# Kernel optimization log

Measured on AMD Instinct MI355X. Metric: run time of the kernel, lower is better.

## Reference

```python
import jax, jax.numpy as jnp
import numpy as np

B, N, E = 2, 50000, 800000
INP, KEY, VAL = 128, 64, 128
LN_EPS = 1e-5


def setup_inputs() -> dict:
    key = jax.random.key(0)
    ks = jax.random.split(key, 12)
    s_in = 1.0 / np.sqrt(INP).astype(np.float32)
    s_val = 1.0 / np.sqrt(VAL).astype(np.float32)
    return {
        "x": jax.random.normal(ks[0], (B, N, INP), jnp.float32),
        "conn_vals": jax.random.uniform(ks[1], (E,), jnp.float32),
        "k_w": jax.random.normal(ks[2], (INP, KEY), jnp.float32) * s_in,
        "k_b": jax.random.normal(ks[3], (KEY,), jnp.float32) * 0.01,
        "v_w": jax.random.normal(ks[4], (INP, VAL), jnp.float32) * s_in,
        "v_b": jax.random.normal(ks[5], (VAL,), jnp.float32) * 0.01,
        "out_w": jax.random.normal(ks[6], (VAL, VAL), jnp.float32) * s_val,
        "out_b": jax.random.normal(ks[7], (VAL,), jnp.float32) * 0.01,
        "ln_g": jnp.ones((VAL,), jnp.float32),
        "ln_b": jnp.zeros((VAL,), jnp.float32),
        "rows": jax.random.randint(ks[8], (E,), 0, N),
        "cols": jax.random.randint(ks[9], (E,), 0, N),
    }


def reference(x, conn_vals, k_w, k_b, v_w, v_b, out_w, out_b, ln_g, ln_b, rows, cols):
    # x: [B, N, INP]; edge list (rows -> receivers, cols -> senders)
    keys = x @ k_w + k_b                      # [B, N, KEY]
    values = x @ v_w + v_b                    # [B, N, VAL]

    # weights[i, j, b] = conn[i, j] * sum_k keys[b, j, k]
    ksum = keys.sum(axis=-1)                  # [B, N]
    score = conn_vals[:, None] * ksum[:, cols].T   # [E, B]

    # sparse softmax over dim=1 (senders j), per receiver row i and batch b,
    # restricted to specified (edge) entries only
    m = jax.ops.segment_max(score, rows, num_segments=N)     # [N, B]
    m = jnp.where(jnp.isfinite(m), m, 0.0)                   # empty rows
    ex = jnp.exp(score - m[rows])                            # [E, B]
    denom = jax.ops.segment_sum(ex, rows, num_segments=N)    # [N, B]
    w = ex / jnp.where(denom == 0.0, 1.0, denom)[rows]       # [E, B]

    # output[i, b, :] = sum_j w[i, j, b] * values[b, j, :]
    vals_g = jnp.swapaxes(values[:, cols], 0, 1)             # [E, B, VAL]
    msgs = w[:, :, None] * vals_g                            # [E, B, VAL]
    agg = jax.ops.segment_sum(msgs, rows, num_segments=N)    # [N, B, VAL]

    h = jnp.transpose(agg, (1, 0, 2)) @ out_w + out_b        # [B, N, VAL]
    h = jax.nn.silu(h)

    mu = h.mean(axis=-1, keepdims=True)
    var = ((h - mu) ** 2).mean(axis=-1, keepdims=True)
    out = (h - mu) / jnp.sqrt(var + LN_EPS) * ln_g + ln_b
    return out
```

## Files before the change

### kernel.cpp

```cpp
#include <hip/hip_runtime.h>
#include <hip/hip_bf16.h>

#define NB    2
#define NNODE 50000
#define NEDGE 800000
#define INPD  128
#define KEYD  64
#define VALD  128
#define MTOT  (NB * NNODE)
#define VBLK  3125
#define EPT   16
#define SBLK  ((NEDGE + 256 * EPT - 1) / (256 * EPT))
#define ECAP  80

typedef __attribute__((ext_vector_type(8))) short bf16x8;
typedef __attribute__((ext_vector_type(4))) float f32x4;

__device__ __forceinline__ unsigned short f2bf(float f) {
    unsigned u = __float_as_uint(f);
    u += 0x7FFFu + ((u >> 16) & 1u);
    return (unsigned short)(u >> 16);
}

__global__ void prep_kernel(const float* __restrict__ kw, const float* __restrict__ kb,
                            const float* __restrict__ vw, const float* __restrict__ ow,
                            float* __restrict__ kwsum,
                            unsigned short* __restrict__ vwT, unsigned short* __restrict__ owT,
                            int* __restrict__ cursor) {
    int bid = blockIdx.x, tid = threadIdx.x;
    if (bid < 64) {
        int idx = bid * 256 + tid;
        int n = idx >> 7, k = idx & 127;
        vwT[idx] = f2bf(vw[k * VALD + n]);
    } else if (bid < 128) {
        int idx = (bid - 64) * 256 + tid;
        int n = idx >> 7, k = idx & 127;
        owT[idx] = f2bf(ow[k * VALD + n]);
    } else if (bid == 128) {
        if (tid < INPD) {
            float s = 0.f;
            for (int j = 0; j < KEYD; ++j) s += kw[tid * KEYD + j];
            kwsum[tid] = s;
        }
        if (tid == 0) {
            float s = 0.f;
            for (int j = 0; j < KEYD; ++j) s += kb[j];
            kwsum[INPD] = s;
        }
    } else {
        int idx = (bid - 129) * 256 + tid;
        if (idx < NNODE) cursor[idx] = idx * ECAP;
    }
}

__global__ __launch_bounds__(256, 8)
void values_build_kernel(const float* __restrict__ x, const float* __restrict__ vb,
                         const float* __restrict__ kwsum,
                         const unsigned short* __restrict__ vwT,
                         const int* __restrict__ rows_e, const int* __restrict__ cols_e,
                         const float* __restrict__ conn,
                         uint2* __restrict__ values_pk, float* __restrict__ ksum,
                         int* __restrict__ cursor, uint2* __restrict__ edge_s) {
    __shared__ unsigned short xs[32 * 136];
    __shared__ unsigned short pk[16 * 264];
    int tid = threadIdx.x;
    if (blockIdx.x < SBLK) {
        int base = blockIdx.x * 256 + tid;
#pragma unroll
        for (int k = 0; k < EPT; ++k) {
            int e = base + k * (SBLK * 256);
            if (e < NEDGE) {
                int r = rows_e[e];
                int o = atomicAdd(&cursor[r], 1);
                if (o < r * ECAP + ECAP) {
                    unsigned long long pkd =
                        (unsigned long long)(unsigned)cols_e[e]
                        | ((unsigned long long)__float_as_uint(conn[e]) << 32);
                    __builtin_nontemporal_store(
                        pkd, (unsigned long long*)&edge_s[o]);
                }
            }
        }
        return;
    }
    int node0 = (blockIdx.x - SBLK) * 16;

    {
        int row = tid >> 4;
        int cseg = tid & 15;
        const float4* p0 = (const float4*)(x + (size_t)(node0 + row) * INPD) + cseg * 2;
        const float4* p1 = (const float4*)(x + (size_t)(NNODE + node0 + row) * INPD) + cseg * 2;
        float4 u0 = p0[0], u1 = p0[1];
        float4 w0 = p1[0], w1 = p1[1];
        const float4* kwp = (const float4*)kwsum + cseg * 2;
        float4 ka = kwp[0], kc = kwp[1];
        float kp0 = u0.x * ka.x + u0.y * ka.y + u0.z * ka.z + u0.w * ka.w
                  + u1.x * kc.x + u1.y * kc.y + u1.z * kc.z + u1.w * kc.w;
        float kp1 = w0.x * ka.x + w0.y * ka.y + w0.z * ka.z + w0.w * ka.w
                  + w1.x * kc.x + w1.y * kc.y + w1.z * kc.z + w1.w * kc.w;
#pragma unroll
        for (int o = 1; o < 16; o <<= 1) {
            kp0 += __shfl_xor(kp0, o);
            kp1 += __shfl_xor(kp1, o);
        }
        if (cseg == 0) {
            float kb = kwsum[INPD];
            ksum[node0 + row] = kp0 + kb;
            ksum[NNODE + node0 + row] = kp1 + kb;
        }
        union { unsigned short h[8]; uint4 q; } a, b;
        a.h[0] = f2bf(u0.x); a.h[1] = f2bf(u0.y); a.h[2] = f2bf(u0.z); a.h[3] = f2bf(u0.w);
        a.h[4] = f2bf(u1.x); a.h[5] = f2bf(u1.y); a.h[6] = f2bf(u1.z); a.h[7] = f2bf(u1.w);
        b.h[0] = f2bf(w0.x); b.h[1] = f2bf(w0.y); b.h[2] = f2bf(w0.z); b.h[3] = f2bf(w0.w);
        b.h[4] = f2bf(w1.x); b.h[5] = f2bf(w1.y); b.h[6] = f2bf(w1.z); b.h[7] = f2bf(w1.w);
        *(uint4*)(xs + row * 136 + cseg * 8) = a.q;
        *(uint4*)(xs + (16 + row) * 136 + cseg * 8) = b.q;
    }
    __syncthreads();

    int wave = tid >> 6, lane = tid & 63;
    int m = lane & 15, quad = lane >> 4;
    int n0 = wave * 32;
    f32x4 acc00 = {0.f, 0.f, 0.f, 0.f};
    f32x4 acc01 = {0.f, 0.f, 0.f, 0.f};
    f32x4 acc10 = {0.f, 0.f, 0.f, 0.f};
    f32x4 acc11 = {0.f, 0.f, 0.f, 0.f};
    const unsigned short* r0 = xs + m * 136;
    const unsigned short* r1 = xs + (16 + m) * 136;
    const unsigned short* bw0 = vwT + (size_t)(n0 + m) * INPD;
    const unsigned short* bw1 = vwT + (size_t)(n0 + 16 + m) * INPD;
#pragma unroll
    for (int kk = 0; kk < 4; ++kk) {
        int k0 = kk * 32 + quad * 8;
        bf16x8 A0 = *(const bf16x8*)(r0 + k0);
        bf16x8 A1 = *(const bf16x8*)(r1 + k0);
        bf16x8 B0 = *(const bf16x8*)(bw0 + k0);
        bf16x8 B1 = *(const bf16x8*)(bw1 + k0);
        acc00 = __builtin_amdgcn_mfma_f32_16x16x32_bf16(A0, B0, acc00, 0, 0, 0);
        acc01 = __builtin_amdgcn_mfma_f32_16x16x32_bf16(A0, B1, acc01, 0, 0, 0);
        acc10 = __builtin_amdgcn_mfma_f32_16x16x32_bf16(A1, B0, acc10, 0, 0, 0);
        acc11 = __builtin_amdgcn_mfma_f32_16x16x32_bf16(A1, B1, acc11, 0, 0, 0);
    }
    int c0 = n0 + m, c1 = n0 + 16 + m;
    float vb0 = vb[c0], vb1 = vb[c1];
    int p0 = (c0 >> 1) * 4 + (c0 & 1);
    int p1 = (c1 >> 1) * 4 + (c1 & 1);
#pragma unroll
    for (int r = 0; r < 4; ++r) {
        int nl = quad * 4 + r;
        pk[nl * 264 + p0]     = f2bf(acc00[r] + vb0);
        pk[nl * 264 + p0 + 2] = f2bf(acc10[r] + vb0);
        pk[nl * 264 + p1]     = f2bf(acc01[r] + vb1);
        pk[nl * 264 + p1 + 2] = f2bf(acc11[r] + vb1);
    }
    __syncthreads();
    {
        int node = tid >> 4, chunk = tid & 15;
        uint4 q0 = *(const uint4*)(pk + node * 264 + chunk * 8);
        uint4 q1 = *(const uint4*)(pk + node * 264 + (chunk + 16) * 8);
        uint4* dst = (uint4*)((char*)values_pk + (size_t)node0 * 512) + node * 32;
        dst[chunk] = q0;
        dst[chunk + 16] = q1;
    }
}

__global__ __launch_bounds__(256)
void aggregate_kernel(const int* __restrict__ cursor,
                      const uint2* __restrict__ edge_s,
                      const float* __restrict__ ksum,
                      const uint2* __restrict__ values_pk,
                      unsigned short* __restrict__ agg_bf) {
    int wave = threadIdx.x >> 6, lane = threadIdx.x & 63;
    int wid = blockIdx.x * 4 + wave;
    for (int rr = 0; rr < 2; ++rr) {
        int i = wid * 2 + rr;
        if (i >= NNODE) break;
        int start = i * ECAP;
        int len = min(cursor[i] - start, ECAP);
        float acc00 = 0.f, acc01 = 0.f, acc10 = 0.f, acc11 = 0.f;
        if (len > 0) {
            if (len <= 64) {
                float ex0 = 0.f, ex1 = 0.f; int colv = 0;
                if (lane < len) {
                    uint2 e = edge_s[start + lane];
                    colv = (int)e.x;
                    float cv = __uint_as_float(e.y);
                    ex0 = __expf(cv * ksum[colv]);
                    ex1 = __expf(cv * ksum[NNODE + colv]);
                }
                float s0 = ex0, s1 = ex1;
#pragma unroll
                for (int o = 1; o < 64; o <<= 1) { s0 += __shfl_xor(s0, o); s1 += __shfl_xor(s1, o); }
                float inv0 = 1.0f / s0, inv1 = 1.0f / s1;
                int p = 0;
                for (; p + 3 < len; p += 4) {
                    int c0 = __shfl(colv, p),     c1 = __shfl(colv, p + 1);
                    int c2 = __shfl(colv, p + 2), c3 = __shfl(colv, p + 3);
                    float wa0 = __shfl(ex0, p) * inv0,     wb0 = __shfl(ex1, p) * inv1;
                    float wa1 = __shfl(ex0, p + 1) * inv0, wb1 = __shfl(ex1, p + 1) * inv1;
                    float wa2 = __shfl(ex0, p + 2) * inv0, wb2 = __shfl(ex1, p + 2) * inv1;
                    float wa3 = __shfl(ex0, p + 3) * inv0, wb3 = __shfl(ex1, p + 3) * inv1;
                    uint2 v0 = values_pk[(size_t)c0 * 64 + lane];
                    uint2 v1 = values_pk[(size_t)c1 * 64 + lane];
                    uint2 v2 = values_pk[(size_t)c2 * 64 + lane];
                    uint2 v3 = values_pk[(size_t)c3 * 64 + lane];
                    acc00 += wa0 * __uint_as_float(v0.x << 16) + wa1 * __uint_as_float(v1.x << 16)
                           + wa2 * __uint_as_float(v2.x << 16) + wa3 * __uint_as_float(v3.x << 16);
                    acc01 += wa0 * __uint_as_float(v0.x & 0xFFFF0000u) + wa1 * __uint_as_float(v1.x & 0xFFFF0000u)
                           + wa2 * __uint_as_float(v2.x & 0xFFFF0000u) + wa3 * __uint_as_float(v3.x & 0xFFFF0000u);
                    acc10 += wb0 * __uint_as_float(v0.y << 16) + wb1 * __uint_as_float(v1.y << 16)
                           + wb2 * __uint_as_float(v2.y << 16) + wb3 * __uint_as_float(v3.y << 16);
                    acc11 += wb0 * __uint_as_float(v0.y & 0xFFFF0000u) + wb1 * __uint_as_float(v1.y & 0xFFFF0000u)
                           + wb2 * __uint_as_float(v2.y & 0xFFFF0000u) + wb3 * __uint_as_float(v3.y & 0xFFFF0000u);
                }
                for (; p < len; ++p) {
                    int c = __shfl(colv, p);
                    float w0 = __shfl(ex0, p) * inv0;
                    float w1 = __shfl(ex1, p) * inv1;
                    uint2 v = values_pk[(size_t)c * 64 + lane];
                    acc00 += w0 * __uint_as_float(v.x << 16);
                    acc01 += w0 * __uint_as_float(v.x & 0xFFFF0000u);
                    acc10 += w1 * __uint_as_float(v.y << 16);
                    acc11 += w1 * __uint_as_float(v.y & 0xFFFF0000u);
                }
            } else {
                float s0 = 0.f, s1 = 0.f;
                for (int basep = 0; basep < len; basep += 64) {
                    int q = basep + lane;
                    if (q < len) {
                        uint2 e = edge_s[start + q];
                        int c = (int)e.x;
                        float cv = __uint_as_float(e.y);
                        s0 += __expf(cv * ksum[c]);
                        s1 += __expf(cv * ksum[NNODE + c]);
                    }
                }
#pragma unroll
                for (int o = 1; o < 64; o <<= 1) { s0 += __shfl_xor(s0, o); s1 += __shfl_xor(s1, o); }
                float inv0 = 1.0f / s0, inv1 = 1.0f / s1;
                for (int p = 0; p < len; ++p) {
                    uint2 e = edge_s[start + p];
                    int c = (int)e.x;
                    float cv = __uint_as_float(e.y);
                    float w0 = __expf(cv * ksum[c]) * inv0;
                    float w1 = __expf(cv * ksum[NNODE + c]) * inv1;
                    uint2 v = values_pk[(size_t)c * 64 + lane];
                    acc00 += w0 * __uint_as_float(v.x << 16);
                    acc01 += w0 * __uint_as_float(v.x & 0xFFFF0000u);
                    acc10 += w1 * __uint_as_float(v.y << 16);
                    acc11 += w1 * __uint_as_float(v.y & 0xFFFF0000u);
                }
            }
        }
        unsigned o0 = ((unsigned)f2bf(acc01) << 16) | (unsigned)f2bf(acc00);
        unsigned o1 = ((unsigned)f2bf(acc11) << 16) | (unsigned)f2bf(acc10);
        ((unsigned*)(agg_bf + (size_t)i * VALD))[lane] = o0;
        ((unsigned*)(agg_bf + (size_t)(NNODE + i) * VALD))[lane] = o1;
    }
}

__global__ __launch_bounds__(256)
void out_kernel(const unsigned short* __restrict__ agg_bf,
                const unsigned short* __restrict__ owT,
                const float* __restrict__ ob,
                const float* __restrict__ lng, const float* __restrict__ lnb,
                float* __restrict__ out) {
    __shared__ float hs[16][VALD + 2];
    __shared__ float ps[16][16];
    __shared__ float psq[16][16];
    __shared__ float mu_s[16], rs_s[16];
    int m0 = blockIdx.x * 16;
    int tid = threadIdx.x;
    int wave = tid >> 6, lane = tid & 63;
    int m = lane & 15, quad = lane >> 4;
    int n0 = wave * 32;
    f32x4 a0 = {0.f, 0.f, 0.f, 0.f}, a1 = {0.f, 0.f, 0.f, 0.f};
    const unsigned short* arow = agg_bf + (size_t)(m0 + m) * VALD;
#pragma unroll
    for (int kk = 0; kk < 4; ++kk) {
        int k0 = kk * 32 + quad * 8;
        bf16x8 af = *(const bf16x8*)(arow + k0);
        bf16x8 b0 = *(const bf16x8*)(owT + (size_t)(n0 + m) * VALD + k0);
        bf16x8 b1 = *(const bf16x8*)(owT + (size_t)(n0 + 16 + m) * VALD + k0);
        a0 = __builtin_amdgcn_mfma_f32_16x16x32_bf16(af, b0, a0, 0, 0, 0);
        a1 = __builtin_amdgcn_mfma_f32_16x16x32_bf16(af, b1, a1, 0, 0, 0);
    }
#pragma unroll
    for (int r = 0; r < 4; ++r) {
        int row = quad * 4 + r;
        {
            int col = n0 + m;
            float h = a0[r] + ob[col];
            hs[row][col] = h / (1.f + __expf(-h));
        }
        {
            int col = n0 + 16 + m;
            float h = a1[r] + ob[col];
            hs[row][col] = h / (1.f + __expf(-h));
        }
    }
    __syncthreads();
    {
        int row = tid >> 4, seg = tid & 15;
        float s = 0.f, q = 0.f;
#pragma unroll
        for (int j = 0; j < 8; ++j) {
            float v = hs[row][seg * 8 + j];
            s += v; q += v * v;
        }
        ps[row][seg] = s; psq[row][seg] = q;
    }
    __syncthreads();
    if (tid < 16) {
        float s = 0.f, q = 0.f;
#pragma unroll
        for (int j = 0; j < 16; ++j) { s += ps[tid][j]; q += psq[tid][j]; }
        float mu = s * (1.f / 128.f);
        float var = q * (1.f / 128.f) - mu * mu;
        mu_s[tid] = mu;
        rs_s[tid] = rsqrtf(var + 1e-5f);
    }
    __syncthreads();
#pragma unroll
    for (int j = 0; j < 8; ++j) {
        int e = tid + 256 * j;
        int row = e >> 7, col = e & 127;
        out[(size_t)(m0 + row) * VALD + col] =
            (hs[row][col] - mu_s[row]) * rs_s[row] * lng[col] + lnb[col];
    }
}

extern "C" void kernel_launch(void* const* d_in, const int* in_sizes, int n_in,
                              void* d_out, int out_size, void* d_ws, size_t ws_size,
                              hipStream_t stream) {
    (void)in_sizes; (void)n_in; (void)out_size; (void)ws_size;
    const float* x    = (const float*)d_in[0];
    const float* conn = (const float*)d_in[1];
    const float* kw   = (const float*)d_in[2];
    const float* kb   = (const float*)d_in[3];
    const float* vw   = (const float*)d_in[4];
    const float* vb   = (const float*)d_in[5];
    const float* ow   = (const float*)d_in[6];
    const float* ob   = (const float*)d_in[7];
    const float* lng  = (const float*)d_in[8];
    const float* lnb  = (const float*)d_in[9];
    const int* rows   = (const int*)d_in[10];
    const int* cols   = (const int*)d_in[11];
    float* out        = (float*)d_out;

    char* w = (char*)d_ws;
    auto alloc = [&](size_t bytes) {
        char* p = w;
        w += (bytes + 255) & ~(size_t)255;
        return p;
    };
    uint2* values_pk       = (uint2*)alloc((size_t)NNODE * 512);
    unsigned short* agg_bf = (unsigned short*)alloc((size_t)MTOT * VALD * 2);
    float* ksum   = (float*)alloc((size_t)MTOT * 4);
    float* kwsum  = (float*)alloc(256 * 4);
    int*   cursor = (int*)alloc((size_t)NNODE * 4);
    uint2* edge_s = (uint2*)alloc((size_t)NNODE * ECAP * 8);
    unsigned short* vwT = (unsigned short*)alloc((size_t)INPD * VALD * 2);
    unsigned short* owT = (unsigned short*)alloc((size_t)VALD * VALD * 2);

    prep_kernel<<<129 + 196, 256, 0, stream>>>(kw, kb, vw, ow, kwsum, vwT, owT, cursor);
    values_build_kernel<<<SBLK + VBLK, 256, 0, stream>>>(
        x, vb, kwsum, vwT, rows, cols, conn, values_pk, ksum, cursor, edge_s);
    aggregate_kernel<<<(NNODE + 7) / 8, 256, 0, stream>>>(
        cursor, edge_s, ksum, values_pk, agg_bf);
    out_kernel<<<MTOT / 16, 256, 0, stream>>>(agg_bf, owT, ob, lng, lnb, out);
}
```

Before: 264.2 us.

## Fuse aggregation with output projection, SiLU and LayerNorm via shared memory

Merges the aggregate and out kernels so each block aggregates 8 nodes for both batches, stages the bf16 results in LDS as a 16-row tile, then runs the MFMA projection, SiLU and LayerNorm directly. This removes the global round-trip of the aggregated tensor (write then read of roughly 51 MB in bf16) and one kernel launch. In exchange, each block now holds extra LDS and a block-wide barrier after the irregular gather phase, which may reduce occupancy and let slow waves stall the whole block.

Result: faster. 246.1 us, median of 2 (-6.9%).

```diff
diff --git a/kernel.cpp b/kernel.cpp
--- a/kernel.cpp
+++ b/kernel.cpp
@@ -165,16 +165,26 @@
 }
 
 __global__ __launch_bounds__(256)
-void aggregate_kernel(const int* __restrict__ cursor,
-                      const uint2* __restrict__ edge_s,
-                      const float* __restrict__ ksum,
-                      const uint2* __restrict__ values_pk,
-                      unsigned short* __restrict__ agg_bf) {
-    int wave = threadIdx.x >> 6, lane = threadIdx.x & 63;
-    int wid = blockIdx.x * 4 + wave;
+void aggregate_out_kernel(const int* __restrict__ cursor,
+                          const uint2* __restrict__ edge_s,
+                          const float* __restrict__ ksum,
+                          const uint2* __restrict__ values_pk,
+                          const unsigned short* __restrict__ owT,
+                          const float* __restrict__ ob,
+                          const float* __restrict__ lng, const float* __restrict__ lnb,
+                          float* __restrict__ out) {
+    __shared__ unsigned aggL[16 * 68];
+    __shared__ float hs[16][VALD + 2];
+    __shared__ float ps[16][16];
+    __shared__ float psq[16][16];
+    __shared__ float mu_s[16], rs_s[16];
+    int tid = threadIdx.x;
+    int wave = tid >> 6, lane = tid & 63;
+    int node_base = blockIdx.x * 8;
+
     for (int rr = 0; rr < 2; ++rr) {
-        int i = wid * 2 + rr;
-        if (i >= NNODE) break;
+        int nl = wave * 2 + rr;
+        int i = node_base + nl;
         int start = i * ECAP;
         int len = min(cursor[i] - start, ECAP);
         float acc00 = 0.f, acc01 = 0.f, acc10 = 0.f, acc11 = 0.f;
@@ -254,28 +264,15 @@
         }
         unsigned o0 = ((unsigned)f2bf(acc01) << 16) | (unsigned)f2bf(acc00);
         unsigned o1 = ((unsigned)f2bf(acc11) << 16) | (unsigned)f2bf(acc10);
-        ((unsigned*)(agg_bf + (size_t)i * VALD))[lane] = o0;
-        ((unsigned*)(agg_bf + (size_t)(NNODE + i) * VALD))[lane] = o1;
-    }
-}
-
-__global__ __launch_bounds__(256)
-void out_kernel(const unsigned short* __restrict__ agg_bf,
-                const unsigned short* __restrict__ owT,
-                const float* __restrict__ ob,
-                const float* __restrict__ lng, const float* __restrict__ lnb,
-                float* __restrict__ out) {
-    __shared__ float hs[16][VALD + 2];
-    __shared__ float ps[16][16];
-    __shared__ float psq[16][16];
-    __shared__ float mu_s[16], rs_s[16];
-    int m0 = blockIdx.x * 16;
-    int tid = threadIdx.x;
-    int wave = tid >> 6, lane = tid & 63;
+        aggL[nl * 68 + lane]       = o0;
+        aggL[(8 + nl) * 68 + lane] = o1;
+    }
+    __syncthreads();
+
     int m = lane & 15, quad = lane >> 4;
     int n0 = wave * 32;
     f32x4 a0 = {0.f, 0.f, 0.f, 0.f}, a1 = {0.f, 0.f, 0.f, 0.f};
-    const unsigned short* arow = agg_bf + (size_t)(m0 + m) * VALD;
+    const unsigned short* arow = (const unsigned short*)aggL + m * 136;
 #pragma unroll
     for (int kk = 0; kk < 4; ++kk) {
         int k0 = kk * 32 + quad * 8;
@@ -325,7 +322,9 @@
     for (int j = 0; j < 8; ++j) {
         int e = tid + 256 * j;
         int row = e >> 7, col = e & 127;
-        out[(size_t)(m0 + row) * VALD + col] =
+        size_t grow = (row < 8 ? (size_t)(node_base + row)
+                               : (size_t)NNODE + node_base + (row - 8));
+        out[grow * VALD + col] =
             (hs[row][col] - mu_s[row]) * rs_s[row] * lng[col] + lnb[col];
     }
 }
@@ -354,8 +353,7 @@
         w += (bytes + 255) & ~(size_t)255;
         return p;
     };
-    uint2* values_pk       = (uint2*)alloc((size_t)NNODE * 512);
-    unsigned short* agg_bf = (unsigned short*)alloc((size_t)MTOT * VALD * 2);
+    uint2* values_pk = (uint2*)alloc((size_t)NNODE * 512);
     float* ksum   = (float*)alloc((size_t)MTOT * 4);
     float* kwsum  = (float*)alloc(256 * 4);
     int*   cursor = (int*)alloc((size_t)NNODE * 4);
@@ -366,7 +364,6 @@
     prep_kernel<<<129 + 196, 256, 0, stream>>>(kw, kb, vw, ow, kwsum, vwT, owT, cursor);
     values_build_kernel<<<SBLK + VBLK, 256, 0, stream>>>(
         x, vb, kwsum, vwT, rows, cols, conn, values_pk, ksum, cursor, edge_s);
-    aggregate_kernel<<<(NNODE + 7) / 8, 256, 0, stream>>>(
-        cursor, edge_s, ksum, values_pk, agg_bf);
-    out_kernel<<<MTOT / 16, 256, 0, stream>>>(agg_bf, owT, ob, lng, lnb, out);
-}
+    aggregate_out_kernel<<<NNODE / 8, 256, 0, stream>>>(
+        cursor, edge_s, ksum, values_pk, owT, ob, lng, lnb, out);
+}
```
